# Kernel tuning notes

Hardware: AMD Instinct MI355X
Metric: run time of the kernel (lower is better)

Reference implementation:

```python
import jax, jax.numpy as jnp
import numpy as np

N = 100000  # nodes
EPS_BN = 1e-5
EPS_NORM = 1e-12


def sage_conv(x, edge_index, wl, bl, wr):
    # PyG SAGEConv (aggr='mean', normalize=True, project=False):
    # out = lin_l(mean_{j in N(i)} x_j) + lin_r(x_i); then L2-normalize rows.
    src, dst = edge_index[0], edge_index[1]
    msgs = x[src]                                            # [E, C] gather
    agg = jax.ops.segment_sum(msgs, dst, num_segments=N)     # [N, C]
    cnt = jax.ops.segment_sum(jnp.ones((edge_index.shape[1],), x.dtype), dst,
                              num_segments=N)                # [N]
    agg = agg / jnp.maximum(cnt, 1.0)[:, None]               # mean (0 for isolated)
    out = agg @ wl.T + bl + x @ wr.T                         # lin_l has bias, lin_r doesn't
    nrm = jnp.sqrt(jnp.sum(out * out, axis=-1, keepdims=True))
    return out / jnp.maximum(nrm, EPS_NORM)


def batch_norm(x, gamma, beta):
    # BatchNorm1d in training mode: batch stats, biased variance
    mean = jnp.mean(x, axis=0)
    var = jnp.mean((x - mean) ** 2, axis=0)
    return gamma * (x - mean) * jax.lax.rsqrt(var + EPS_BN) + beta


def setup_inputs() -> dict:
    key = jax.random.key(0)
    ks = jax.random.split(key, 9)
    C_in, C_h, C_out = 128, 128, 47
    E = 800000
    x = jax.random.normal(ks[0], (N, C_in), dtype=jnp.float32)
    edge_index = jax.random.randint(ks[1], (2, E), 0, N, dtype=jnp.int64)
    s = 0.1
    return {
        "x": x,
        "edge_index": edge_index,
        "w1l": jax.random.normal(ks[2], (C_h, C_in), dtype=jnp.float32) * s,
        "b1l": jnp.zeros((C_h,), dtype=jnp.float32),
        "w1r": jax.random.normal(ks[3], (C_h, C_in), dtype=jnp.float32) * s,
        "bn_gamma": jnp.ones((C_h,), dtype=jnp.float32),
        "bn_beta": jnp.zeros((C_h,), dtype=jnp.float32),
        "w2l": jax.random.normal(ks[4], (C_out, C_h), dtype=jnp.float32) * s,
        "b2l": jnp.zeros((C_out,), dtype=jnp.float32),
        "w2r": jax.random.normal(ks[5], (C_out, C_h), dtype=jnp.float32) * s,
    }


def reference(x, edge_index, w1l, b1l, w1r, bn_gamma, bn_beta, w2l, b2l, w2r):
    h = sage_conv(x, edge_index, w1l, b1l, w1r)   # [N, 128]
    h = batch_norm(h, bn_gamma, bn_beta)
    h = jax.nn.relu(h)
    # dropout p=0.0 -> identity
    out = sage_conv(h, edge_index, w2l, b2l, w2r)  # [N, 47]
    return out
```

## Files before the change

### kernel.cpp

```cpp
#include <hip/hip_runtime.h>
#include <cstdint>


typedef __attribute__((ext_vector_type(8))) short s8v;
typedef __attribute__((ext_vector_type(4))) short s4v;
typedef __attribute__((ext_vector_type(4))) float fx4;

#define CSR_CHUNK 8192
#define CSR_SH 8
#define CSR_NBPAD 512
#define CSR_BUFCAP 3072

static __device__ __forceinline__ float bf2f(unsigned short h) {
    union { unsigned int u; float f; } c; c.u = (unsigned int)h << 16; return c.f;
}
static __device__ __forceinline__ unsigned short f2bf(float f) {
    union { float f; unsigned int u; } c; c.f = f;
    unsigned int u = c.u;
    return (unsigned short)((u + 0x7FFF + ((u >> 16) & 1)) >> 16);
}

__global__ __launch_bounds__(256) void k_prep(
        const float* __restrict__ x, const float* __restrict__ w1l,
        const float* __restrict__ w1r, const float* __restrict__ w2l,
        const float* __restrict__ w2r, const int* __restrict__ ei,
        unsigned short* __restrict__ xb, unsigned short* __restrict__ wB1,
        unsigned short* __restrict__ wB2p, float* __restrict__ stats,
        int* __restrict__ counts, int n, int nE, int prepBlocks) {
    __shared__ int hist[CSR_NBPAD];
    int t = threadIdx.x;
    if ((int)blockIdx.x >= prepBlocks) {
        int chunk = blockIdx.x - prepBlocks;
        hist[t] = 0; hist[t + 256] = 0;
        __syncthreads();
        int e0 = chunk * CSR_CHUNK;
        int e1 = min(e0 + CSR_CHUNK, nE);
        for (int e = e0 + t; e < e1; e += 256)
            atomicAdd(&hist[ei[nE + e] >> CSR_SH], 1);
        __syncthreads();
        counts[chunk * CSR_NBPAD + t] = hist[t];
        counts[chunk * CSR_NBPAD + t + 256] = hist[t + 256];
        return;
    }
    int idx = blockIdx.x * 256 + t;
    int nx = n * 16;
    if (idx < nx) {
        float4 a = ((const float4*)x)[idx * 2];
        float4 b = ((const float4*)x)[idx * 2 + 1];
        union { s8v v; unsigned short u[8]; } o;
        o.u[0] = f2bf(a.x); o.u[1] = f2bf(a.y); o.u[2] = f2bf(a.z); o.u[3] = f2bf(a.w);
        o.u[4] = f2bf(b.x); o.u[5] = f2bf(b.y); o.u[6] = f2bf(b.z); o.u[7] = f2bf(b.w);
        ((s8v*)xb)[idx] = o.v;
        return;
    }
    idx -= nx;
    if (idx < 32768) {
        int j = idx >> 8, k = idx & 255;
        float v = (k < 128) ? w1l[j * 128 + k] : w1r[j * 128 + (k - 128)];
        wB1[idx] = f2bf(v);
        return;
    }
    idx -= 32768;
    if (idx < 16384) {
        int j = idx >> 7, k = idx & 127;
        float v = 0.f;
        if (j < 47)      v = w2l[j * 128 + k];
        else if (j < 94) v = w2r[(j - 47) * 128 + k];
        wB2p[idx] = f2bf(v);
        return;
    }
    idx -= 16384;
    if (idx < 256) stats[idx] = 0.f;
}

__global__ __launch_bounds__(256) void k_bmeta(
        const int* __restrict__ counts, int* __restrict__ bucketStart,
        int* __restrict__ gcur, int nCh, int NB) {
    __shared__ int tot[CSR_NBPAD], tot2[CSR_NBPAD], sh[256], bs[CSR_NBPAD];
    int t = threadIdx.x;
    int tl = t & 127, g = t >> 7;
    int half = (nCh + 1) >> 1;
    int c0 = g * half, c1 = min(nCh, c0 + half);
    int4 s4 = {0, 0, 0, 0};
    for (int c = c0; c < c1; ++c) {
        int4 v = *(const int4*)(counts + (size_t)c * CSR_NBPAD + tl * 4);
        s4.x += v.x; s4.y += v.y; s4.z += v.z; s4.w += v.w;
    }
    *(int4*)((g ? tot2 : tot) + tl * 4) = s4;
    __syncthreads();
    tot[t] += tot2[t];
    tot[t + 256] += tot2[t + 256];
    __syncthreads();
    int pairSum = tot[2 * t] + tot[2 * t + 1];
    sh[t] = pairSum;
    __syncthreads();
    for (int off = 1; off < 256; off <<= 1) {
        int add = (t >= off) ? sh[t - off] : 0;
        __syncthreads();
        sh[t] += add;
        __syncthreads();
    }
    int excl = sh[t] - pairSum;
    bs[2 * t] = excl;
    bs[2 * t + 1] = excl + tot[2 * t];
    __syncthreads();
    for (int b = t; b <= NB; b += 256) bucketStart[b] = bs[b];
    for (int b = t; b < CSR_NBPAD; b += 256) gcur[b] = bs[b];
}

__global__ __launch_bounds__(256) void k_bfill(
        const int* __restrict__ ei, const int* __restrict__ counts,
        int* __restrict__ gcur, int* __restrict__ pairs, int nE) {
    __shared__ int cur[CSR_NBPAD];
    int t = threadIdx.x;
    #pragma unroll
    for (int i = 0; i < 2; ++i) {
        int b = t + i * 256;
        int h = counts[blockIdx.x * CSR_NBPAD + b];
        cur[b] = h ? atomicAdd(&gcur[b], h) : 0;
    }
    __syncthreads();
    int e0 = blockIdx.x * CSR_CHUNK;
    int e1 = min(e0 + CSR_CHUNK, nE);
    for (int e = e0 + t; e < e1; e += 256) {
        int s = ei[e];
        int d = ei[nE + e];
        int p = atomicAdd(&cur[d >> CSR_SH], 1);
        pairs[p] = (s << 8) | (d & 255);
    }
}

__global__ __launch_bounds__(256) void k_csr(
        const int* __restrict__ pairs, const int* __restrict__ bucketStart,
        int* __restrict__ deg, int* __restrict__ rowStart,
        int* __restrict__ srcIdx, int n) {
    __shared__ int cnt[256], scn[256], cur[256];
    __shared__ int buf[CSR_BUFCAP];
    int t = threadIdx.x;
    int bkt = blockIdx.x;
    int eBeg = bucketStart[bkt], eEnd = bucketStart[bkt + 1];
    int node0 = bkt << CSR_SH;
    cnt[t] = 0;
    __syncthreads();
    for (int e = eBeg + t; e < eEnd; e += 256)
        atomicAdd(&cnt[pairs[e] & 255], 1);
    __syncthreads();
    int myc = cnt[t];
    scn[t] = myc;
    __syncthreads();
    for (int off = 1; off < 256; off <<= 1) {
        int add = (t >= off) ? scn[t - off] : 0;
        __syncthreads();
        scn[t] += add;
        __syncthreads();
    }
    int excl = scn[t] - myc;
    cur[t] = excl;
    int node = node0 + t;
    if (node < n) { deg[node] = myc; rowStart[node] = eBeg + excl; }
    __syncthreads();
    for (int e = eBeg + t; e < eEnd; e += 256) {
        int pk = pairs[e];
        int p = atomicAdd(&cur[pk & 255], 1);
        int src = pk >> 8;
        if (p < CSR_BUFCAP) buf[p] = src;
        else srcIdx[eBeg + p] = src;
    }
    __syncthreads();
    int m = min(eEnd - eBeg, CSR_BUFCAP);
    for (int i = t; i < m; i += 256) srcIdx[eBeg + i] = buf[i];
}

__global__ __launch_bounds__(256) void k_gather1(
        const unsigned short* __restrict__ xb, const int* __restrict__ rowStart,
        const int* __restrict__ deg, const int* __restrict__ srcIdx,
        unsigned short* __restrict__ aggb, int n) {
    int t = threadIdx.x;
    int q = t & 15, grp = t >> 4;
    int node = blockIdx.x * 16 + grp;
    if (node >= n) return;
    int beg = rowStart[node];
    int d = deg[node];
    int end = beg + d;
    float a0[8] = {}, a1[8] = {}, a2[8] = {}, a3[8] = {};
    int e = beg;
    for (; e + 4 <= end; e += 4) {
        int s0 = srcIdx[e], s1v = srcIdx[e + 1], s2 = srcIdx[e + 2], s3 = srcIdx[e + 3];
        s8v v0 = *(const s8v*)(xb + (size_t)s0 * 128 + q * 8);
        s8v v1 = *(const s8v*)(xb + (size_t)s1v * 128 + q * 8);
        s8v v2 = *(const s8v*)(xb + (size_t)s2 * 128 + q * 8);
        s8v v3 = *(const s8v*)(xb + (size_t)s3 * 128 + q * 8);
        #pragma unroll
        for (int u = 0; u < 8; ++u) {
            a0[u] += bf2f((unsigned short)v0[u]);
            a1[u] += bf2f((unsigned short)v1[u]);
            a2[u] += bf2f((unsigned short)v2[u]);
            a3[u] += bf2f((unsigned short)v3[u]);
        }
    }
    for (; e < end; ++e) {
        s8v v0 = *(const s8v*)(xb + (size_t)srcIdx[e] * 128 + q * 8);
        #pragma unroll
        for (int u = 0; u < 8; ++u) a0[u] += bf2f((unsigned short)v0[u]);
    }
    float ic = 1.0f / fmaxf((float)d, 1.0f);
    union { s8v v; unsigned short u[8]; } o;
    #pragma unroll
    for (int u = 0; u < 8; ++u)
        o.u[u] = f2bf((a0[u] + a1[u] + a2[u] + a3[u]) * ic);
    *(s8v*)(aggb + (size_t)node * 128 + q * 8) = o.v;
}

#define GLL16(GSRC, LDST) \
    __builtin_amdgcn_global_load_lds( \
        (__attribute__((address_space(1))) void*)(void*)(GSRC), \
        (__attribute__((address_space(3))) void*)(LDST), 16, 0, 0)

__global__ __launch_bounds__(256, 3) void k_gemm1(
        const unsigned short* __restrict__ xb, const unsigned short* __restrict__ aggb,
        const unsigned short* __restrict__ wB1, const float* __restrict__ b1l,
        unsigned short* __restrict__ s1b, float* __restrict__ stats, int n) {
    __shared__ __align__(16) unsigned short xs[128 * 32];
    __shared__ __align__(16) unsigned short ws[128 * 32];
    int t = threadIdx.x;
    int w = t >> 6, L = t & 63;
    int q = L >> 4, lm = L & 15;
    int wr0 = (w >> 1) * 64;
    int wc0 = (w & 1) * 64;
    int r0 = blockIdx.x * 128;

    fx4 acc[4][4];
    fx4 z4 = {0.f, 0.f, 0.f, 0.f};
    #pragma unroll
    for (int r = 0; r < 4; ++r)
        #pragma unroll
        for (int c = 0; c < 4; ++c) acc[r][c] = z4;

    for (int kt = 0; kt < 8; ++kt) {
        const unsigned short* src = (kt < 4) ? aggb : xb;
        int kbase = (kt & 3) * 32;
        __syncthreads();
        #pragma unroll
        for (int it = 0; it < 2; ++it) {
            int i = t + it * 256;
            int row = i >> 2, p = i & 3;
            int sl = p ^ ((row >> 1) & 3);
            int gr = r0 + row; gr = gr < n ? gr : (n - 1);
            GLL16(src + (size_t)gr * 128 + kbase + sl * 8, &xs[i * 8]);
            GLL16(wB1 + (size_t)row * 256 + kt * 32 + sl * 8, &ws[i * 8]);
        }
        __syncthreads();
        s8v af[4], bfr[4];
        #pragma unroll
        for (int r = 0; r < 4; ++r) {
            int row = wr0 + r * 16 + lm;
            af[r] = *(const s8v*)&xs[row * 32 + ((q ^ ((row >> 1) & 3)) << 3)];
        }
        #pragma unroll
        for (int c = 0; c < 4; ++c) {
            int row = wc0 + c * 16 + lm;
            bfr[c] = *(const s8v*)&ws[row * 32 + ((q ^ ((row >> 1) & 3)) << 3)];
        }
        #pragma unroll
        for (int r = 0; r < 4; ++r)
            #pragma unroll
            for (int c = 0; c < 4; ++c)
                acc[r][c] = __builtin_amdgcn_mfma_f32_16x16x32_bf16(af[r], bfr[c], acc[r][c], 0, 0, 0);
    }

    float bj[4];
    #pragma unroll
    for (int c = 0; c < 4; ++c) bj[c] = b1l[wc0 + c * 16 + lm];
    #pragma unroll
    for (int r = 0; r < 4; ++r)
        #pragma unroll
        for (int c = 0; c < 4; ++c) acc[r][c] += bj[c];

    fx4 pr[4];
    #pragma unroll
    for (int r = 0; r < 4; ++r) {
        fx4 p = acc[r][0] * acc[r][0];
        #pragma unroll
        for (int c = 1; c < 4; ++c) p += acc[r][c] * acc[r][c];
        #pragma unroll
        for (int off = 1; off <= 8; off <<= 1)
            #pragma unroll
            for (int i2 = 0; i2 < 4; ++i2) p[i2] += __shfl_xor(p[i2], off, 64);
        pr[r] = p;
    }

    __syncthreads();
    float* norm2 = (float*)xs;
    float* invn  = (float*)xs + 256;
    float* statS = (float*)ws;
    float* statQ = (float*)ws + 256;
    if (lm == 0) {
        #pragma unroll
        for (int r = 0; r < 4; ++r)
            #pragma unroll
            for (int i = 0; i < 4; ++i)
                norm2[(wr0 + r * 16 + q * 4 + i) * 2 + (w & 1)] = pr[r][i];
    }
    __syncthreads();
    if (t < 128) {
        float s = norm2[t * 2] + norm2[t * 2 + 1];
        invn[t] = 1.0f / fmaxf(sqrtf(s), 1e-12f);
    }
    __syncthreads();

    float cS[4] = {}, cQ[4] = {};
    #pragma unroll
    for (int r = 0; r < 4; ++r) {
        int rowb = wr0 + r * 16 + q * 4;
        fx4 iv = *(const fx4*)&invn[rowb];
        #pragma unroll
        for (int c = 0; c < 4; ++c) {
            fx4 v = acc[r][c] * iv;
            int col = wc0 + c * 16 + lm;
            #pragma unroll
            for (int i = 0; i < 4; ++i) {
                int gr = r0 + rowb + i;
                if (gr < n) {
                    s1b[(size_t)gr * 128 + col] = f2bf(v[i]);
                    cS[c] += v[i];
                    cQ[c] += v[i] * v[i];
                }
            }
        }
    }
    #pragma unroll
    for (int off = 16; off <= 32; off <<= 1)
        #pragma unroll
        for (int c = 0; c < 4; ++c) {
            cS[c] += __shfl_xor(cS[c], off, 64);
            cQ[c] += __shfl_xor(cQ[c], off, 64);
        }
    if (q == 0) {
        #pragma unroll
        for (int c = 0; c < 4; ++c) {
            int col = wc0 + c * 16 + lm;
            statS[col * 2 + (w >> 1)] = cS[c];
            statQ[col * 2 + (w >> 1)] = cQ[c];
        }
    }
    __syncthreads();
    if (t < 128) {
        atomicAdd(&stats[t],       statS[t * 2] + statS[t * 2 + 1]);
        atomicAdd(&stats[128 + t], statQ[t * 2] + statQ[t * 2 + 1]);
    }
}

__global__ __launch_bounds__(256, 3) void k_gemm2(
        const unsigned short* __restrict__ s1b, const unsigned short* __restrict__ wB2p,
        const float* __restrict__ stats, const float* __restrict__ gamma,
        const float* __restrict__ beta, const float* __restrict__ b2l,
        unsigned short* __restrict__ y2b, float* __restrict__ rbuf, int n) {
    __shared__ __align__(16) unsigned short xs[128 * 32];
    __shared__ __align__(16) unsigned short ws[128 * 32];
    __shared__ __align__(16) float abuf[128];
    __shared__ __align__(16) float bbuf[128];
    int t = threadIdx.x;
    int w = t >> 6, L = t & 63;
    int q = L >> 4, lm = L & 15;
    int wr0 = (w >> 1) * 64, wc0 = (w & 1) * 64;
    int r0 = blockIdx.x * 128;

    if (t < 128) {
        float s = stats[t], qv = stats[128 + t];
        float fn = (float)n;
        float mean = s / fn;
        float var = qv / fn - mean * mean;
        float istd = rsqrtf(var + 1e-5f);
        float a = gamma[t] * istd;
        abuf[t] = a;
        bbuf[t] = beta[t] - mean * a;
    }
    __syncthreads();

    fx4 acc[4][4];
    fx4 z4 = {0.f, 0.f, 0.f, 0.f};
    #pragma unroll
    for (int r = 0; r < 4; ++r)
        #pragma unroll
        for (int c = 0; c < 4; ++c) acc[r][c] = z4;

    for (int kt = 0; kt < 4; ++kt) {
        int kbase = kt * 32;
        __syncthreads();
        #pragma unroll
        for (int it = 0; it < 2; ++it) {
            int i = t + it * 256;
            int row = i >> 2, p = i & 3;
            int sl = p ^ ((row >> 1) & 3);
            int gr = r0 + row; gr = gr < n ? gr : (n - 1);
            GLL16(s1b + (size_t)gr * 128 + kbase + sl * 8, &xs[i * 8]);
            GLL16(wB2p + (size_t)row * 128 + kbase + sl * 8, &ws[i * 8]);
        }
        __syncthreads();
        fx4 a0 = *(const fx4*)&abuf[kbase + q * 8];
        fx4 a1 = *(const fx4*)&abuf[kbase + q * 8 + 4];
        fx4 b0 = *(const fx4*)&bbuf[kbase + q * 8];
        fx4 b1 = *(const fx4*)&bbuf[kbase + q * 8 + 4];
        s8v af[4], bfr[4];
        #pragma unroll
        for (int r = 0; r < 4; ++r) {
            int row = wr0 + r * 16 + lm;
            s8v sv = *(const s8v*)&xs[row * 32 + ((q ^ ((row >> 1) & 3)) << 3)];
            union { s8v v; unsigned short u[8]; } o;
            #pragma unroll
            for (int u = 0; u < 4; ++u) {
                float h0 = fmaxf(fmaf(a0[u], bf2f((unsigned short)sv[u]), b0[u]), 0.f);
                float h1 = fmaxf(fmaf(a1[u], bf2f((unsigned short)sv[u + 4]), b1[u]), 0.f);
                o.u[u]     = f2bf(h0);
                o.u[u + 4] = f2bf(h1);
            }
            af[r] = o.v;
        }
        #pragma unroll
        for (int c = 0; c < 4; ++c) {
            int row = wc0 + c * 16 + lm;
            bfr[c] = *(const s8v*)&ws[row * 32 + ((q ^ ((row >> 1) & 3)) << 3)];
        }
        #pragma unroll
        for (int r = 0; r < 4; ++r)
            #pragma unroll
            for (int c = 0; c < 4; ++c)
                acc[r][c] = __builtin_amdgcn_mfma_f32_16x16x32_bf16(af[r], bfr[c], acc[r][c], 0, 0, 0);
    }

    #pragma unroll
    for (int c = 0; c < 4; ++c) {
        int col = wc0 + c * 16 + lm;
        float bb = (col >= 47 && col < 94) ? b2l[col - 47] : 0.f;
        #pragma unroll
        for (int r = 0; r < 4; ++r) {
            int rowb = wr0 + r * 16 + q * 4;
            #pragma unroll
            for (int i = 0; i < 4; ++i) {
                int gr = r0 + rowb + i;
                if (gr >= n) continue;
                float v = acc[r][c][i];
                if (col < 47)      y2b[(size_t)gr * 64 + col] = f2bf(v);
                else if (col < 94) rbuf[(size_t)gr * 48 + (col - 47)] = v + bb;
            }
        }
    }
}

__global__ __launch_bounds__(256) void k_gather2_final(
        const unsigned short* __restrict__ y2b, const float* __restrict__ rbuf,
        const int* __restrict__ rowStart, const int* __restrict__ deg,
        const int* __restrict__ srcIdx, float* __restrict__ out, int n) {
    int t = threadIdx.x;
    int q = t & 15, grp = t >> 4;
    int node = blockIdx.x * 16 + grp;
    if (node >= n) return;
    int beg = rowStart[node];
    int d = deg[node];
    int end = beg + d;
    float acc[4] = {0.f, 0.f, 0.f, 0.f};
    int e = beg;
    for (; e + 8 <= end; e += 8) {
        int s0 = srcIdx[e],     s1v = srcIdx[e + 1];
        int s2 = srcIdx[e + 2], s3  = srcIdx[e + 3];
        int s4 = srcIdx[e + 4], s5  = srcIdx[e + 5];
        int s6 = srcIdx[e + 6], s7  = srcIdx[e + 7];
        s4v v0 = *(const s4v*)(y2b + (size_t)s0 * 64 + q * 4);
        s4v v1 = *(const s4v*)(y2b + (size_t)s1v * 64 + q * 4);
        s4v v2 = *(const s4v*)(y2b + (size_t)s2 * 64 + q * 4);
        s4v v3 = *(const s4v*)(y2b + (size_t)s3 * 64 + q * 4);
        s4v v4 = *(const s4v*)(y2b + (size_t)s4 * 64 + q * 4);
        s4v v5 = *(const s4v*)(y2b + (size_t)s5 * 64 + q * 4);
        s4v v6 = *(const s4v*)(y2b + (size_t)s6 * 64 + q * 4);
        s4v v7 = *(const s4v*)(y2b + (size_t)s7 * 64 + q * 4);
        #pragma unroll
        for (int u = 0; u < 4; ++u) {
            acc[u] += (bf2f((unsigned short)v0[u]) + bf2f((unsigned short)v1[u]))
                    + (bf2f((unsigned short)v2[u]) + bf2f((unsigned short)v3[u]))
                    + (bf2f((unsigned short)v4[u]) + bf2f((unsigned short)v5[u]))
                    + (bf2f((unsigned short)v6[u]) + bf2f((unsigned short)v7[u]));
        }
    }
    for (; e + 4 <= end; e += 4) {
        int s0 = srcIdx[e],     s1v = srcIdx[e + 1];
        int s2 = srcIdx[e + 2], s3  = srcIdx[e + 3];
        s4v v0 = *(const s4v*)(y2b + (size_t)s0 * 64 + q * 4);
        s4v v1 = *(const s4v*)(y2b + (size_t)s1v * 64 + q * 4);
        s4v v2 = *(const s4v*)(y2b + (size_t)s2 * 64 + q * 4);
        s4v v3 = *(const s4v*)(y2b + (size_t)s3 * 64 + q * 4);
        #pragma unroll
        for (int u = 0; u < 4; ++u)
            acc[u] += (bf2f((unsigned short)v0[u]) + bf2f((unsigned short)v1[u]))
                    + (bf2f((unsigned short)v2[u]) + bf2f((unsigned short)v3[u]));
    }
    for (; e < end; ++e) {
        s4v v0 = *(const s4v*)(y2b + (size_t)srcIdx[e] * 64 + q * 4);
        #pragma unroll
        for (int u = 0; u < 4; ++u) acc[u] += bf2f((unsigned short)v0[u]);
    }
    float ic = 1.0f / fmaxf((float)d, 1.0f);
    fx4 rb = *(const fx4*)(rbuf + (size_t)node * 48 + q * 4);
    float vi[4];
    float ss = 0.f;
    #pragma unroll
    for (int u = 0; u < 4; ++u) {
        int ch = q * 4 + u;
        float v = (ch < 47) ? (acc[u] * ic + rb[u]) : 0.f;
        vi[u] = v;
        ss += v * v;
    }
    #pragma unroll
    for (int off = 1; off <= 8; off <<= 1) ss += __shfl_xor(ss, off, 64);
    float inv = 1.0f / fmaxf(sqrtf(ss), 1e-12f);
    #pragma unroll
    for (int u = 0; u < 4; ++u) {
        int ch = q * 4 + u;
        if (ch < 47) out[(size_t)node * 47 + ch] = vi[u] * inv;
    }
}

extern "C" void kernel_launch(void* const* d_in, const int* in_sizes, int n_in,
                              void* d_out, int out_size, void* d_ws, size_t ws_size,
                              hipStream_t stream) {
    const float* x     = (const float*)d_in[0];
    const int*   ei    = (const int*)d_in[1];
    const float* w1l   = (const float*)d_in[2];
    const float* b1l   = (const float*)d_in[3];
    const float* w1r   = (const float*)d_in[4];
    const float* gamma = (const float*)d_in[5];
    const float* beta  = (const float*)d_in[6];
    const float* w2l   = (const float*)d_in[7];
    const float* b2l   = (const float*)d_in[8];
    const float* w2r   = (const float*)d_in[9];
    float* out = (float*)d_out;

    int n  = in_sizes[0] / 128;
    int nE = in_sizes[1] / 2;

    int NB  = (n + 255) >> 8;
    int nCh = (nE + CSR_CHUNK - 1) / CSR_CHUNK;

    int* deg       = (int*)d_ws;
    float* stats   = (float*)(deg + n);
    int* rowStart  = (int*)(stats + 256);
    int* meta      = rowStart + n;
    int* srcIdx    = meta + n;
    unsigned short* xb   = (unsigned short*)(srcIdx + nE);
    unsigned short* aggb = xb + (size_t)n * 128;
    unsigned short* s1b  = aggb + (size_t)n * 128;
    unsigned short* wB1  = s1b + (size_t)n * 128;
    unsigned short* wB2p = wB1 + 32768;
    int* counts      = meta;
    int* bucketStart = meta + 60000;
    int* gcur        = meta + 61000;
    int* pairs       = (int*)s1b;
    unsigned short* y2b = xb;
    float* rbuf = (float*)(y2b + (size_t)n * 64);

    int prepTotal  = n * 16 + 32768 + 16384 + 256;
    int prepBlocks = (prepTotal + 255) / 256;

    k_prep<<<prepBlocks + nCh, 256, 0, stream>>>(
        x, w1l, w1r, w2l, w2r, ei, xb, wB1, wB2p, stats, counts, n, nE, prepBlocks);
    k_bmeta<<<1, 256, 0, stream>>>(counts, bucketStart, gcur, nCh, NB);
    k_bfill<<<nCh, 256, 0, stream>>>(ei, counts, gcur, pairs, nE);
    k_csr<<<NB, 256, 0, stream>>>(pairs, bucketStart, deg, rowStart, srcIdx, n);
    k_gather1<<<(n + 15) / 16, 256, 0, stream>>>(xb, rowStart, deg, srcIdx, aggb, n);
    k_gemm1<<<(n + 127) / 128, 256, 0, stream>>>(xb, aggb, wB1, b1l, s1b, stats, n);
    k_gemm2<<<(n + 127) / 128, 256, 0, stream>>>(
        s1b, wB2p, stats, gamma, beta, b2l, y2b, rbuf, n);
    k_gather2_final<<<(n + 15) / 16, 256, 0, stream>>>(y2b, rbuf, rowStart, deg, srcIdx, out, n);
}
```

Baseline: 270.1 us.

## Load GEMM MFMA operands directly from global memory instead of LDS staging

Both GEMM kernels stop staging A and B tiles through shared memory with global_load_lds and barriers. Each lane now loads its MFMA fragments straight from global memory (L2/L1), with the k-loop fully unrolled so loads can be issued early. This removes the LDS round trip and the per-iteration __syncthreads, but each fragment is fetched twice (by two waves) through cache, and the loads are 16-byte strided rows rather than coalesced tiles.

Measured after the change: 298.7 us. 10.6% more time.

```diff
diff --git a/kernel.cpp b/kernel.cpp
--- a/kernel.cpp
+++ b/kernel.cpp
@@ -211,17 +211,14 @@
     *(s8v*)(aggb + (size_t)node * 128 + q * 8) = o.v;
 }
 
-#define GLL16(GSRC, LDST) \
-    __builtin_amdgcn_global_load_lds( \
-        (__attribute__((address_space(1))) void*)(void*)(GSRC), \
-        (__attribute__((address_space(3))) void*)(LDST), 16, 0, 0)
-
 __global__ __launch_bounds__(256, 3) void k_gemm1(
         const unsigned short* __restrict__ xb, const unsigned short* __restrict__ aggb,
         const unsigned short* __restrict__ wB1, const float* __restrict__ b1l,
         unsigned short* __restrict__ s1b, float* __restrict__ stats, int n) {
-    __shared__ __align__(16) unsigned short xs[128 * 32];
-    __shared__ __align__(16) unsigned short ws[128 * 32];
+    __shared__ float norm2[256];
+    __shared__ float invn[128];
+    __shared__ float statS[256];
+    __shared__ float statQ[256];
     int t = threadIdx.x;
     int w = t >> 6, L = t & 63;
     int q = L >> 4, lm = L & 15;
@@ -229,6 +226,14 @@
     int wc0 = (w & 1) * 64;
     int r0 = blockIdx.x * 128;
 
+    int arow[4], brow[4];
+    #pragma unroll
+    for (int r = 0; r < 4; ++r) {
+        int gr = r0 + wr0 + r * 16 + lm;
+        arow[r] = gr < n ? gr : (n - 1);
+        brow[r] = wc0 + r * 16 + lm;
+    }
+
     fx4 acc[4][4];
     fx4 z4 = {0.f, 0.f, 0.f, 0.f};
     #pragma unroll
@@ -236,31 +241,17 @@
         #pragma unroll
         for (int c = 0; c < 4; ++c) acc[r][c] = z4;
 
+    #pragma unroll
     for (int kt = 0; kt < 8; ++kt) {
         const unsigned short* src = (kt < 4) ? aggb : xb;
-        int kbase = (kt & 3) * 32;
-        __syncthreads();
-        #pragma unroll
-        for (int it = 0; it < 2; ++it) {
-            int i = t + it * 256;
-            int row = i >> 2, p = i & 3;
-            int sl = p ^ ((row >> 1) & 3);
-            int gr = r0 + row; gr = gr < n ? gr : (n - 1);
-            GLL16(src + (size_t)gr * 128 + kbase + sl * 8, &xs[i * 8]);
-            GLL16(wB1 + (size_t)row * 256 + kt * 32 + sl * 8, &ws[i * 8]);
-        }
-        __syncthreads();
+        int kb = (kt & 3) * 32 + q * 8;
         s8v af[4], bfr[4];
         #pragma unroll
-        for (int r = 0; r < 4; ++r) {
-            int row = wr0 + r * 16 + lm;
-            af[r] = *(const s8v*)&xs[row * 32 + ((q ^ ((row >> 1) & 3)) << 3)];
-        }
-        #pragma unroll
-        for (int c = 0; c < 4; ++c) {
-            int row = wc0 + c * 16 + lm;
-            bfr[c] = *(const s8v*)&ws[row * 32 + ((q ^ ((row >> 1) & 3)) << 3)];
-        }
+        for (int r = 0; r < 4; ++r)
+            af[r] = *(const s8v*)(src + (size_t)arow[r] * 128 + kb);
+        #pragma unroll
+        for (int c = 0; c < 4; ++c)
+            bfr[c] = *(const s8v*)(wB1 + (size_t)brow[c] * 256 + kt * 32 + q * 8);
         #pragma unroll
         for (int r = 0; r < 4; ++r)
             #pragma unroll
@@ -289,11 +280,6 @@
         pr[r] = p;
     }
 
-    __syncthreads();
-    float* norm2 = (float*)xs;
-    float* invn  = (float*)xs + 256;
-    float* statS = (float*)ws;
-    float* statQ = (float*)ws + 256;
     if (lm == 0) {
         #pragma unroll
         for (int r = 0; r < 4; ++r)
@@ -355,8 +341,6 @@
         const float* __restrict__ stats, const float* __restrict__ gamma,
         const float* __restrict__ beta, const float* __restrict__ b2l,
         unsigned short* __restrict__ y2b, float* __restrict__ rbuf, int n) {
-    __shared__ __align__(16) unsigned short xs[128 * 32];
-    __shared__ __align__(16) unsigned short ws[128 * 32];
     __shared__ __align__(16) float abuf[128];
     __shared__ __align__(16) float bbuf[128];
     int t = threadIdx.x;
@@ -377,6 +361,14 @@
     }
     __syncthreads();
 
+    int arow[4], brow[4];
+    #pragma unroll
+    for (int r = 0; r < 4; ++r) {
+        int gr = r0 + wr0 + r * 16 + lm;
+        arow[r] = gr < n ? gr : (n - 1);
+        brow[r] = wc0 + r * 16 + lm;
+    }
+
     fx4 acc[4][4];
     fx4 z4 = {0.f, 0.f, 0.f, 0.f};
     #pragma unroll
@@ -384,28 +376,17 @@
         #pragma unroll
         for (int c = 0; c < 4; ++c) acc[r][c] = z4;
 
+    #pragma unroll
     for (int kt = 0; kt < 4; ++kt) {
-        int kbase = kt * 32;
-        __syncthreads();
-        #pragma unroll
-        for (int it = 0; it < 2; ++it) {
-            int i = t + it * 256;
-            int row = i >> 2, p = i & 3;
-            int sl = p ^ ((row >> 1) & 3);
-            int gr = r0 + row; gr = gr < n ? gr : (n - 1);
-            GLL16(s1b + (size_t)gr * 128 + kbase + sl * 8, &xs[i * 8]);
-            GLL16(wB2p + (size_t)row * 128 + kbase + sl * 8, &ws[i * 8]);
-        }
-        __syncthreads();
-        fx4 a0 = *(const fx4*)&abuf[kbase + q * 8];
-        fx4 a1 = *(const fx4*)&abuf[kbase + q * 8 + 4];
-        fx4 b0 = *(const fx4*)&bbuf[kbase + q * 8];
-        fx4 b1 = *(const fx4*)&bbuf[kbase + q * 8 + 4];
+        int kb = kt * 32 + q * 8;
+        fx4 a0 = *(const fx4*)&abuf[kb];
+        fx4 a1 = *(const fx4*)&abuf[kb + 4];
+        fx4 b0 = *(const fx4*)&bbuf[kb];
+        fx4 b1 = *(const fx4*)&bbuf[kb + 4];
         s8v af[4], bfr[4];
         #pragma unroll
         for (int r = 0; r < 4; ++r) {
-            int row = wr0 + r * 16 + lm;
-            s8v sv = *(const s8v*)&xs[row * 32 + ((q ^ ((row >> 1) & 3)) << 3)];
+            s8v sv = *(const s8v*)(s1b + (size_t)arow[r] * 128 + kb);
             union { s8v v; unsigned short u[8]; } o;
             #pragma unroll
             for (int u = 0; u < 4; ++u) {
@@ -417,10 +398,8 @@
             af[r] = o.v;
         }
         #pragma unroll
-        for (int c = 0; c < 4; ++c) {
-            int row = wc0 + c * 16 + lm;
-            bfr[c] = *(const s8v*)&ws[row * 32 + ((q ^ ((row >> 1) & 3)) << 3)];
-        }
+        for (int c = 0; c < 4; ++c)
+            bfr[c] = *(const s8v*)(wB2p + (size_t)brow[c] * 128 + kb);
         #pragma unroll
         for (int r = 0; r < 4; ++r)
             #pragma unroll
```

## Halve GEMM row tiles to 64 and spread BN stat atomics over 8 slots

Applied to the files above, without the earlier changes.

Both GEMM kernels now use 64-row tiles instead of 128, with each wave computing 2x4 MFMA tiles. This doubles the block count (about 1563 vs 782) and raises the occupancy hint to 4 blocks per SIMD-unit group, which should fill the 256 CUs better. The BatchNorm sum and sum-of-squares atomics in gemm1 are spread over 8 copies indexed by blockIdx to cut contention, and gemm2 adds the copies back together. The cost is that the weight tile is loaded from global memory twice as often per output row, and the stats workspace grows.

Result: faster. 261.8 us (-3.1%).

```diff
diff --git a/kernel.cpp b/kernel.cpp
--- a/kernel.cpp
+++ b/kernel.cpp
@@ -70,7 +70,7 @@
         return;
     }
     idx -= 16384;
-    if (idx < 256) stats[idx] = 0.f;
+    if (idx < 2048) stats[idx] = 0.f;
 }
 
 __global__ __launch_bounds__(256) void k_bmeta(
@@ -216,23 +216,27 @@
         (__attribute__((address_space(1))) void*)(void*)(GSRC), \
         (__attribute__((address_space(3))) void*)(LDST), 16, 0, 0)
 
-__global__ __launch_bounds__(256, 3) void k_gemm1(
+__global__ __launch_bounds__(256, 4) void k_gemm1(
         const unsigned short* __restrict__ xb, const unsigned short* __restrict__ aggb,
         const unsigned short* __restrict__ wB1, const float* __restrict__ b1l,
         unsigned short* __restrict__ s1b, float* __restrict__ stats, int n) {
-    __shared__ __align__(16) unsigned short xs[128 * 32];
+    __shared__ __align__(16) unsigned short xs[64 * 32];
     __shared__ __align__(16) unsigned short ws[128 * 32];
+    __shared__ float norm2[128];
+    __shared__ float invn[64];
+    __shared__ float statS[256];
+    __shared__ float statQ[256];
     int t = threadIdx.x;
     int w = t >> 6, L = t & 63;
     int q = L >> 4, lm = L & 15;
-    int wr0 = (w >> 1) * 64;
+    int wr0 = (w >> 1) * 32;
     int wc0 = (w & 1) * 64;
-    int r0 = blockIdx.x * 128;
-
-    fx4 acc[4][4];
+    int r0 = blockIdx.x * 64;
+
+    fx4 acc[2][4];
     fx4 z4 = {0.f, 0.f, 0.f, 0.f};
     #pragma unroll
-    for (int r = 0; r < 4; ++r)
+    for (int r = 0; r < 2; ++r)
         #pragma unroll
         for (int c = 0; c < 4; ++c) acc[r][c] = z4;
 
@@ -240,19 +244,23 @@
         const unsigned short* src = (kt < 4) ? aggb : xb;
         int kbase = (kt & 3) * 32;
         __syncthreads();
-        #pragma unroll
-        for (int it = 0; it < 2; ++it) {
-            int i = t + it * 256;
-            int row = i >> 2, p = i & 3;
+        {
+            int row = t >> 2, p = t & 3;
             int sl = p ^ ((row >> 1) & 3);
             int gr = r0 + row; gr = gr < n ? gr : (n - 1);
-            GLL16(src + (size_t)gr * 128 + kbase + sl * 8, &xs[i * 8]);
-            GLL16(wB1 + (size_t)row * 256 + kt * 32 + sl * 8, &ws[i * 8]);
-        }
-        __syncthreads();
-        s8v af[4], bfr[4];
-        #pragma unroll
-        for (int r = 0; r < 4; ++r) {
+            GLL16(src + (size_t)gr * 128 + kbase + sl * 8, &xs[t * 8]);
+            #pragma unroll
+            for (int it = 0; it < 2; ++it) {
+                int i = t + it * 256;
+                int wrow = i >> 2, wp = i & 3;
+                int wsl = wp ^ ((wrow >> 1) & 3);
+                GLL16(wB1 + (size_t)wrow * 256 + kt * 32 + wsl * 8, &ws[i * 8]);
+            }
+        }
+        __syncthreads();
+        s8v af[2], bfr[4];
+        #pragma unroll
+        for (int r = 0; r < 2; ++r) {
             int row = wr0 + r * 16 + lm;
             af[r] = *(const s8v*)&xs[row * 32 + ((q ^ ((row >> 1) & 3)) << 3)];
         }
@@ -262,7 +270,7 @@
             bfr[c] = *(const s8v*)&ws[row * 32 + ((q ^ ((row >> 1) & 3)) << 3)];
         }
         #pragma unroll
-        for (int r = 0; r < 4; ++r)
+        for (int r = 0; r < 2; ++r)
             #pragma unroll
             for (int c = 0; c < 4; ++c)
                 acc[r][c] = __builtin_amdgcn_mfma_f32_16x16x32_bf16(af[r], bfr[c], acc[r][c], 0, 0, 0);
@@ -272,13 +280,13 @@
     #pragma unroll
     for (int c = 0; c < 4; ++c) bj[c] = b1l[wc0 + c * 16 + lm];
     #pragma unroll
-    for (int r = 0; r < 4; ++r)
+    for (int r = 0; r < 2; ++r)
         #pragma unroll
         for (int c = 0; c < 4; ++c) acc[r][c] += bj[c];
 
-    fx4 pr[4];
-    #pragma unroll
-    for (int r = 0; r < 4; ++r) {
+    fx4 pr[2];
+    #pragma unroll
+    for (int r = 0; r < 2; ++r) {
         fx4 p = acc[r][0] * acc[r][0];
         #pragma unroll
         for (int c = 1; c < 4; ++c) p += acc[r][c] * acc[r][c];
@@ -290,19 +298,15 @@
     }
 
     __syncthreads();
-    float* norm2 = (float*)xs;
-    float* invn  = (float*)xs + 256;
-    float* statS = (float*)ws;
-    float* statQ = (float*)ws + 256;
     if (lm == 0) {
         #pragma unroll
-        for (int r = 0; r < 4; ++r)
+        for (int r = 0; r < 2; ++r)
             #pragma unroll
             for (int i = 0; i < 4; ++i)
                 norm2[(wr0 + r * 16 + q * 4 + i) * 2 + (w & 1)] = pr[r][i];
     }
     __syncthreads();
-    if (t < 128) {
+    if (t < 64) {
         float s = norm2[t * 2] + norm2[t * 2 + 1];
         invn[t] = 1.0f / fmaxf(sqrtf(s), 1e-12f);
     }
@@ -310,7 +314,7 @@
 
     float cS[4] = {}, cQ[4] = {};
     #pragma unroll
-    for (int r = 0; r < 4; ++r) {
+    for (int r = 0; r < 2; ++r) {
         int rowb = wr0 + r * 16 + q * 4;
         fx4 iv = *(const fx4*)&invn[rowb];
         #pragma unroll
@@ -345,28 +349,34 @@
     }
     __syncthreads();
     if (t < 128) {
-        atomicAdd(&stats[t],       statS[t * 2] + statS[t * 2 + 1]);
-        atomicAdd(&stats[128 + t], statQ[t * 2] + statQ[t * 2 + 1]);
-    }
-}
-
-__global__ __launch_bounds__(256, 3) void k_gemm2(
+        float* sp = stats + ((int)blockIdx.x & 7) * 256;
+        atomicAdd(&sp[t],       statS[t * 2] + statS[t * 2 + 1]);
+        atomicAdd(&sp[128 + t], statQ[t * 2] + statQ[t * 2 + 1]);
+    }
+}
+
+__global__ __launch_bounds__(256, 4) void k_gemm2(
         const unsigned short* __restrict__ s1b, const unsigned short* __restrict__ wB2p,
         const float* __restrict__ stats, const float* __restrict__ gamma,
         const float* __restrict__ beta, const float* __restrict__ b2l,
         unsigned short* __restrict__ y2b, float* __restrict__ rbuf, int n) {
-    __shared__ __align__(16) unsigned short xs[128 * 32];
+    __shared__ __align__(16) unsigned short xs[64 * 32];
     __shared__ __align__(16) unsigned short ws[128 * 32];
     __shared__ __align__(16) float abuf[128];
     __shared__ __align__(16) float bbuf[128];
     int t = threadIdx.x;
     int w = t >> 6, L = t & 63;
     int q = L >> 4, lm = L & 15;
-    int wr0 = (w >> 1) * 64, wc0 = (w & 1) * 64;
-    int r0 = blockIdx.x * 128;
+    int wr0 = (w >> 1) * 32, wc0 = (w & 1) * 64;
+    int r0 = blockIdx.x * 64;
 
     if (t < 128) {
-        float s = stats[t], qv = stats[128 + t];
+        float s = 0.f, qv = 0.f;
+        #pragma unroll
+        for (int k = 0; k < 8; ++k) {
+            s  += stats[k * 256 + t];
+            qv += stats[k * 256 + 128 + t];
+        }
         float fn = (float)n;
         float mean = s / fn;
         float var = qv / fn - mean * mean;
@@ -377,33 +387,38 @@
     }
     __syncthreads();
 
-    fx4 acc[4][4];
+    fx4 acc[2][4];
     fx4 z4 = {0.f, 0.f, 0.f, 0.f};
     #pragma unroll
-    for (int r = 0; r < 4; ++r)
+    for (int r = 0; r < 2; ++r)
         #pragma unroll
         for (int c = 0; c < 4; ++c) acc[r][c] = z4;
 
     for (int kt = 0; kt < 4; ++kt) {
         int kbase = kt * 32;
         __syncthreads();
-        #pragma unroll
-        for (int it = 0; it < 2; ++it) {
-            int i = t + it * 256;
-            int row = i >> 2, p = i & 3;
+        {
+            int row = t >> 2, p = t & 3;
             int sl = p ^ ((row >> 1) & 3);
             int gr = r0 + row; gr = gr < n ? gr : (n - 1);
-            GLL16(s1b + (size_t)gr * 128 + kbase + sl * 8, &xs[i * 8]);
-            GLL16(wB2p + (size_t)row * 128 + kbase + sl * 8, &ws[i * 8]);
-        }
-        __syncthreads();
-        fx4 a0 = *(const fx4*)&abuf[kbase + q * 8];
-        fx4 a1 = *(const fx4*)&abuf[kbase + q * 8 + 4];
-        fx4 b0 = *(const fx4*)&bbuf[kbase + q * 8];
-        fx4 b1 = *(const fx4*)&bbuf[kbase + q * 8 + 4];
-        s8v af[4], bfr[4];
-        #pragma unroll
-        for (int r = 0; r < 4; ++r) {
+            GLL16(s1b + (size_t)gr * 128 + kbase + sl * 8, &xs[t * 8]);
+            #pragma unroll
+            for (int it = 0; it < 2; ++it) {
+                int i = t + it * 256;
+                int wrow = i >> 2, wp = i & 3;
+                int wsl = wp ^ ((wrow >> 1) & 3);
+                GLL16(wB2p + (size_t)wrow * 128 + kbase + wsl * 8, &ws[i * 8]);
+            }
+        }
+        __syncthreads();
+        int kb = kbase + q * 8;
+        fx4 a0 = *(const fx4*)&abuf[kb];
+        fx4 a1 = *(const fx4*)&abuf[kb + 4];
+        fx4 b0 = *(const fx4*)&bbuf[kb];
+        fx4 b1 = *(const fx4*)&bbuf[kb + 4];
+        s8v af[2], bfr[4];
+        #pragma unroll
+        for (int r = 0; r < 2; ++r) {
             int row = wr0 + r * 16 + lm;
             s8v sv = *(const s8v*)&xs[row * 32 + ((q ^ ((row >> 1) & 3)) << 3)];
             union { s8v v; unsigned short u[8]; } o;
@@ -422,7 +437,7 @@
             bfr[c] = *(const s8v*)&ws[row * 32 + ((q ^ ((row >> 1) & 3)) << 3)];
         }
         #pragma unroll
-        for (int r = 0; r < 4; ++r)
+        for (int r = 0; r < 2; ++r)
             #pragma unroll
             for (int c = 0; c < 4; ++c)
                 acc[r][c] = __builtin_amdgcn_mfma_f32_16x16x32_bf16(af[r], bfr[c], acc[r][c], 0, 0, 0);
@@ -433,7 +448,7 @@
         int col = wc0 + c * 16 + lm;
         float bb = (col >= 47 && col < 94) ? b2l[col - 47] : 0.f;
         #pragma unroll
-        for (int r = 0; r < 4; ++r) {
+        for (int r = 0; r < 2; ++r) {
             int rowb = wr0 + r * 16 + q * 4;
             #pragma unroll
             for (int i = 0; i < 4; ++i) {
@@ -542,7 +557,7 @@
 
     int* deg       = (int*)d_ws;
     float* stats   = (float*)(deg + n);
-    int* rowStart  = (int*)(stats + 256);
+    int* rowStart  = (int*)(stats + 2048);
     int* meta      = rowStart + n;
     int* srcIdx    = meta + n;
     unsigned short* xb   = (unsigned short*)(srcIdx + nE);
@@ -557,7 +572,7 @@
     unsigned short* y2b = xb;
     float* rbuf = (float*)(y2b + (size_t)n * 64);
 
-    int prepTotal  = n * 16 + 32768 + 16384 + 256;
+    int prepTotal  = n * 16 + 32768 + 16384 + 2048;
     int prepBlocks = (prepTotal + 255) / 256;
 
     k_prep<<<prepBlocks + nCh, 256, 0, stream>>>(
@@ -566,8 +581,8 @@
     k_bfill<<<nCh, 256, 0, stream>>>(ei, counts, gcur, pairs, nE);
     k_csr<<<NB, 256, 0, stream>>>(pairs, bucketStart, deg, rowStart, srcIdx, n);
     k_gather1<<<(n + 15) / 16, 256, 0, stream>>>(xb, rowStart, deg, srcIdx, aggb, n);
-    k_gemm1<<<(n + 127) / 128, 256, 0, stream>>>(xb, aggb, wB1, b1l, s1b, stats, n);
-    k_gemm2<<<(n + 127) / 128, 256, 0, stream>>>(
+    k_gemm1<<<(n + 63) / 64, 256, 0, stream>>>(xb, aggb, wB1, b1l, s1b, stats, n);
+    k_gemm2<<<(n + 63) / 64, 256, 0, stream>>>(
         s1b, wB2p, stats, gamma, beta, b2l, y2b, rbuf, n);
     k_gather2_final<<<(n + 15) / 16, 256, 0, stream>>>(y2b, rbuf, rowStart, deg, srcIdx, out, n);
 }
```
